# Kernel tuning notes

Measured on AMD Instinct MI355X. Metric: run time of the kernel, lower is better.

The kernel has to match this reference:

```python
import jax, jax.numpy as jnp
import numpy as np

N = 50000
E = 800000
NEG_SLOPE = 0.2


def gatv2_layer(x, src, dst, Wl, Wr, att, bias, heads, ch):
    # x: [N, Fin]; Wl/Wr: [Fin, heads*ch]; att: [heads, ch]; bias: [heads*ch]
    xl = (x @ Wl).reshape(N, heads, ch)  # source transform
    xr = (x @ Wr).reshape(N, heads, ch)  # target transform
    e = xl[src] + xr[dst]                              # [E, H, C]
    s = jnp.einsum('ehc,hc->eh', jax.nn.leaky_relu(e, NEG_SLOPE), att)  # [E, H]
    # scatter-softmax over incoming edges of each target node
    smax = jax.ops.segment_max(s, dst, num_segments=N)  # [N, H]
    ex = jnp.exp(s - smax[dst])
    denom = jax.ops.segment_sum(ex, dst, num_segments=N)
    alpha = ex / denom[dst]                             # [E, H]
    out = jax.ops.segment_sum(xl[src] * alpha[..., None], dst, num_segments=N)  # [N, H, C]
    return out.reshape(N, heads * ch) + bias


def setup_inputs() -> dict:
    key = jax.random.key(0)
    ks = jax.random.split(key, 12)
    x = jax.random.normal(ks[0], (N, 128), dtype=jnp.float32)
    edge_index = jax.random.randint(ks[1], (2, E), 0, N, dtype=jnp.int64)
    edge_attr = jax.random.normal(ks[2], (E, 16), dtype=jnp.float32)
    s1 = 1.0 / np.sqrt(128.0)
    # layer 1: 128 -> 64, heads=2 (concat -> 128)
    Wl1 = jax.random.normal(ks[3], (128, 128), dtype=jnp.float32) * s1
    Wr1 = jax.random.normal(ks[4], (128, 128), dtype=jnp.float32) * s1
    att1 = jax.random.normal(ks[5], (2, 64), dtype=jnp.float32) * 0.1
    b1 = jnp.zeros((128,), dtype=jnp.float32)
    # layer 2: 128 -> 128, heads=1
    Wl2 = jax.random.normal(ks[6], (128, 128), dtype=jnp.float32) * s1
    Wr2 = jax.random.normal(ks[7], (128, 128), dtype=jnp.float32) * s1
    att2 = jax.random.normal(ks[8], (1, 128), dtype=jnp.float32) * 0.1
    b2 = jnp.zeros((128,), dtype=jnp.float32)
    return {"x": x, "edge_index": edge_index, "edge_attr": edge_attr,
            "Wl1": Wl1, "Wr1": Wr1, "att1": att1, "b1": b1,
            "Wl2": Wl2, "Wr2": Wr2, "att2": att2, "b2": b2}


def reference(x, edge_index, edge_attr, Wl1, Wr1, att1, b1, Wl2, Wr2, att2, b2):
    # using_edge_attr=False default path: edge_attr ignored.
    # GATv2Conv default add_self_loops=True
    loops = jnp.arange(N, dtype=edge_index.dtype)
    src = jnp.concatenate([edge_index[0], loops])
    dst = jnp.concatenate([edge_index[1], loops])
    h = gatv2_layer(x, src, dst, Wl1, Wr1, att1, b1, heads=2, ch=64)
    out = gatv2_layer(h, src, dst, Wl2, Wr2, att2, b2, heads=1, ch=128)
    return out
```

## Files before the change

### kernel.cpp

```cpp
#include <hip/hip_runtime.h>

#define NEG_SLOPE 0.2f
#define NPB 256
#define CHUNK 4096

typedef _Float16 f16x8 __attribute__((ext_vector_type(8)));
typedef _Float16 f16x4 __attribute__((ext_vector_type(4)));
typedef _Float16 f16x2 __attribute__((ext_vector_type(2)));
typedef float    f32x4 __attribute__((ext_vector_type(4)));

__device__ __forceinline__ float lrelu(float v) { return fmaxf(v, NEG_SLOPE * v); }

__device__ __forceinline__ float4 ldf16x4(const _Float16* p) {
    f16x4 v = *(const f16x4*)p;
    return make_float4((float)v[0], (float)v[1], (float)v[2], (float)v[3]);
}

__global__ __launch_bounds__(256) void wsplit_kernel(
    const float* __restrict__ W0, const float* __restrict__ W1,
    const float* __restrict__ W2, const float* __restrict__ W3,
    _Float16* __restrict__ wt)
{
    int idx = blockIdx.x * 256 + threadIdx.x;
    int m = idx >> 14;
    int k = (idx >> 7) & 127;
    int n = idx & 127;
    const float* W = (m == 0) ? W0 : (m == 1) ? W1 : (m == 2) ? W2 : W3;
    wt[m * 16384 + n * 128 + k] = (_Float16)W[k * 128 + n];
}

__global__ __launch_bounds__(256) void xsplit_kernel(
    const float* __restrict__ x, _Float16* __restrict__ xh,
    _Float16* __restrict__ xlo, int total)
{
    int i = blockIdx.x * 256 + threadIdx.x;
    if (i * 2 < total) {
        float2 f = *(const float2*)(x + (size_t)i * 2);
        _Float16 h0 = (_Float16)f.x, h1 = (_Float16)f.y;
        _Float16 l0 = (_Float16)(f.x - (float)h0), l1 = (_Float16)(f.y - (float)h1);
        *(f16x2*)(xh  + (size_t)i * 2) = (f16x2){h0, h1};
        *(f16x2*)(xlo + (size_t)i * 2) = (f16x2){l0, l1};
    }
}

__global__ __launch_bounds__(256) void gemm_f16_kernel(
    const _Float16* __restrict__ Ahi, const _Float16* __restrict__ Alo,
    const _Float16* __restrict__ Wt0, const _Float16* __restrict__ Wt1,
    _Float16* __restrict__ Cl, float* __restrict__ Cr, int N)
{
    const _Float16* Wt = blockIdx.y ? Wt1 : Wt0;

    __shared__ _Float16 ldsW[128 * 136];

    const int tid = threadIdx.x;
    {
        int n = tid >> 1, hf = tid & 1;
        const float4* g = (const float4*)(Wt + n * 128 + hf * 64);
        float4* d = (float4*)&ldsW[n * 136 + hf * 64];
#pragma unroll
        for (int j = 0; j < 8; j++) d[j] = g[j];
    }

    const int wave = tid >> 6;
    const int lane = tid & 63;
    const int mrow = lane & 15;
    const int quad = lane >> 4;
    const int rbase = blockIdx.x * 128 + wave * 32;

    f16x8 ah[2][4], al[2][4];
#pragma unroll
    for (int rt = 0; rt < 2; rt++) {
        int r = rbase + rt * 16 + mrow;
        if (r > N - 1) r = N - 1;
        const _Float16* pa = Ahi + (size_t)r * 128 + quad * 8;
        const _Float16* pl = Alo + (size_t)r * 128 + quad * 8;
#pragma unroll
        for (int s = 0; s < 4; s++) {
            ah[rt][s] = *(const f16x8*)(pa + s * 32);
            al[rt][s] = *(const f16x8*)(pl + s * 32);
        }
    }

    f32x4 acc[2][8];
#pragma unroll
    for (int rt = 0; rt < 2; rt++)
#pragma unroll
        for (int c = 0; c < 8; c++) acc[rt][c] = (f32x4){0.f, 0.f, 0.f, 0.f};

    __syncthreads();

#pragma unroll
    for (int s = 0; s < 4; s++) {
#pragma unroll
        for (int c = 0; c < 8; c++) {
            f16x8 bw = *(const f16x8*)&ldsW[(c * 16 + mrow) * 136 + s * 32 + quad * 8];
            acc[0][c] = __builtin_amdgcn_mfma_f32_16x16x32_f16(ah[0][s], bw, acc[0][c], 0, 0, 0);
            acc[0][c] = __builtin_amdgcn_mfma_f32_16x16x32_f16(al[0][s], bw, acc[0][c], 0, 0, 0);
            acc[1][c] = __builtin_amdgcn_mfma_f32_16x16x32_f16(ah[1][s], bw, acc[1][c], 0, 0, 0);
            acc[1][c] = __builtin_amdgcn_mfma_f32_16x16x32_f16(al[1][s], bw, acc[1][c], 0, 0, 0);
        }
    }

    if (blockIdx.y == 0) {
#pragma unroll
        for (int rt = 0; rt < 2; rt++)
#pragma unroll
            for (int i = 0; i < 4; i++) {
                int r = rbase + rt * 16 + quad * 4 + i;
                if (r < N) {
                    _Float16* cr = Cl + (size_t)r * 128 + mrow;
#pragma unroll
                    for (int c = 0; c < 8; c++) cr[c * 16] = (_Float16)acc[rt][c][i];
                }
            }
    } else {
#pragma unroll
        for (int rt = 0; rt < 2; rt++)
#pragma unroll
            for (int i = 0; i < 4; i++) {
                int r = rbase + rt * 16 + quad * 4 + i;
                if (r < N) {
                    float* cr = Cr + (size_t)r * 128 + mrow;
#pragma unroll
                    for (int c = 0; c < 8; c++) cr[c * 16] = acc[rt][c][i];
                }
            }
    }
}

__global__ __launch_bounds__(256) void histB_kernel(
    const int* __restrict__ ei, int* __restrict__ bcnt, int E)
{
    __shared__ int bh[256];
    int t = threadIdx.x;
    bh[t] = 0;
    __syncthreads();
    int base = blockIdx.x * CHUNK;
#pragma unroll
    for (int j = 0; j < CHUNK / 256; j++) {
        int e = base + t + j * 256;
        if (e < E) atomicAdd(&bh[ei[E + e] >> 8], 1);
    }
    __syncthreads();
    if (bh[t]) atomicAdd(&bcnt[t], bh[t]);
}

__global__ __launch_bounds__(256) void scanB_kernel(
    const int* __restrict__ bcnt, int* __restrict__ bstart,
    int* __restrict__ gcursor, int NB, int E)
{
    __shared__ int s[256];
    int t = threadIdx.x;
    int v = (t < NB) ? bcnt[t] : 0;
    s[t] = v;
    __syncthreads();
    for (int off = 1; off < 256; off <<= 1) {
        int u = (t >= off) ? s[t - off] : 0;
        __syncthreads();
        s[t] += u;
        __syncthreads();
    }
    if (t < NB) { bstart[t] = s[t] - v; gcursor[t] = s[t] - v; }
    if (t == 0) bstart[NB] = E;
}

__global__ __launch_bounds__(256) void passA_kernel(
    const int* __restrict__ ei, int* __restrict__ gcursor,
    int2* __restrict__ staging, int E)
{
    __shared__ int bh[256];
    __shared__ int bbase[256];
    int t = threadIdx.x;
    bh[t] = 0;
    __syncthreads();
    int base = blockIdx.x * CHUNK;
    int srcv[16], dstv[16], rb[16];
#pragma unroll
    for (int j = 0; j < 16; j++) {
        int e = base + t + j * 256;
        if (e < E) {
            int d = ei[E + e];
            srcv[j] = ei[e];
            dstv[j] = d;
            int bk = d >> 8;
            int r = atomicAdd(&bh[bk], 1);
            rb[j] = (r << 8) | bk;
        } else rb[j] = -1;
    }
    __syncthreads();
    if (bh[t]) bbase[t] = atomicAdd(&gcursor[t], bh[t]);
    __syncthreads();
#pragma unroll
    for (int j = 0; j < 16; j++) {
        if (rb[j] >= 0) {
            int bk = rb[j] & 255, r = rb[j] >> 8;
            staging[bbase[bk] + r] = make_int2(srcv[j], dstv[j]);
        }
    }
}

__global__ __launch_bounds__(256) void passB_kernel(
    const int2* __restrict__ staging, const int* __restrict__ bstart,
    int* __restrict__ start, int* __restrict__ sorted_src, int N, int E)
{
    __shared__ int lhist[256], lscan[256], lcur[256];
    int b = blockIdx.x, t = threadIdx.x;
    int r0 = bstart[b], r1 = bstart[b + 1];
    lhist[t] = 0;
    __syncthreads();
    for (int i = r0 + t; i < r1; i += 256) atomicAdd(&lhist[staging[i].y & 255], 1);
    __syncthreads();
    int v = lhist[t];
    lscan[t] = v;
    __syncthreads();
    for (int off = 1; off < 256; off <<= 1) {
        int u = (t >= off) ? lscan[t - off] : 0;
        __syncthreads();
        lscan[t] += u;
        __syncthreads();
    }
    int excl = lscan[t] - v;
    int node = b * NPB + t;
    if (node < N) start[node] = r0 + excl;
    lcur[t] = excl;
    if (b == 0 && t == 0) start[N] = E;
    __syncthreads();
    for (int i = r0 + t; i < r1; i += 256) {
        int2 p = staging[i];
        int rank = atomicAdd(&lcur[p.y & 255], 1);
        sorted_src[r0 + rank] = p.x;
    }
}

template <int H, bool BFOUT>
__global__ __launch_bounds__(256) void gat_fused_kernel(
    const _Float16* __restrict__ xl, const float* __restrict__ xr,
    const float* __restrict__ att, const float* __restrict__ bias,
    const int* __restrict__ start, const int* __restrict__ sorted_src,
    float* __restrict__ outf, _Float16* __restrict__ oh,
    _Float16* __restrict__ ol, int N)
{
    int node = blockIdx.x * 4 + (threadIdx.x >> 6);
    if (node >= N) return;
    const int lane = threadIdx.x & 63;
    const int half = lane >> 5;
    const int hl   = lane & 31;
    const int RED  = (H == 2) ? 8 : 16;

    const float4 b  = *(const float4*)(xr + (size_t)node * 128 + hl * 4);
    const float4 av = *(const float4*)(att + hl * 4);

    float4 acc = make_float4(0.f, 0.f, 0.f, 0.f);
    float den = 0.f;

    const int s0 = start[node];
    const int s1 = start[node + 1];
    const int M  = s1 - s0 + 1;
    const int Ksafe = (M - 1) >> 1;
    const int K     = (M + 1) >> 1;

    int k = 0;
    for (; k + 4 <= Ksafe; k += 4) {
        int src[4];
#pragma unroll
        for (int j = 0; j < 4; j++) {
            int iv = 2 * (k + j) + half;
            src[j] = (iv == 0) ? node : sorted_src[s0 + iv - 1];
        }
        float4 a[4];
#pragma unroll
        for (int j = 0; j < 4; j++)
            a[j] = ldf16x4(xl + (size_t)src[j] * 128 + hl * 4);
        float p[4];
#pragma unroll
        for (int j = 0; j < 4; j++) {
            p[j] = lrelu(a[j].x + b.x) * av.x + lrelu(a[j].y + b.y) * av.y
                 + lrelu(a[j].z + b.z) * av.z + lrelu(a[j].w + b.w) * av.w;
        }
#pragma unroll
        for (int m = 1; m <= RED; m <<= 1) {
#pragma unroll
            for (int j = 0; j < 4; j++) p[j] += __shfl_xor(p[j], m, 64);
        }
#pragma unroll
        for (int j = 0; j < 4; j++) {
            float e = __expf(p[j]);
            den += e;
            acc.x += e * a[j].x; acc.y += e * a[j].y;
            acc.z += e * a[j].z; acc.w += e * a[j].w;
        }
    }
    for (; k < Ksafe; k++) {
        int iv = 2 * k + half;
        int src = (iv == 0) ? node : sorted_src[s0 + iv - 1];
        float4 a = ldf16x4(xl + (size_t)src * 128 + hl * 4);
        float p = lrelu(a.x + b.x) * av.x + lrelu(a.y + b.y) * av.y
                + lrelu(a.z + b.z) * av.z + lrelu(a.w + b.w) * av.w;
#pragma unroll
        for (int m = 1; m <= RED; m <<= 1) p += __shfl_xor(p, m, 64);
        float e = __expf(p);
        den += e;
        acc.x += e * a.x; acc.y += e * a.y; acc.z += e * a.z; acc.w += e * a.w;
    }
    for (; k < K; k++) {
        int iv = 2 * k + half;
        bool valid = iv < M;
        int pos = s0 + (iv > 0 ? iv - 1 : 0);
        int ld = sorted_src[pos];
        int src = (iv == 0) ? node : (valid ? ld : node);
        float4 a = ldf16x4(xl + (size_t)src * 128 + hl * 4);
        float p = lrelu(a.x + b.x) * av.x + lrelu(a.y + b.y) * av.y
                + lrelu(a.z + b.z) * av.z + lrelu(a.w + b.w) * av.w;
#pragma unroll
        for (int m = 1; m <= RED; m <<= 1) p += __shfl_xor(p, m, 64);
        float e = valid ? __expf(p) : 0.f;
        den += e;
        acc.x += e * a.x; acc.y += e * a.y; acc.z += e * a.z; acc.w += e * a.w;
    }

    den   += __shfl_xor(den,   32, 64);
    acc.x += __shfl_xor(acc.x, 32, 64);
    acc.y += __shfl_xor(acc.y, 32, 64);
    acc.z += __shfl_xor(acc.z, 32, 64);
    acc.w += __shfl_xor(acc.w, 32, 64);

    float inv = 1.0f / den;
    float4 bi = *(const float4*)(bias + hl * 4);
    float o0 = acc.x * inv + bi.x;
    float o1 = acc.y * inv + bi.y;
    float o2 = acc.z * inv + bi.z;
    float o3 = acc.w * inv + bi.w;

    if (lane < 32) {
        if (BFOUT) {
            _Float16 h0 = (_Float16)o0, h1 = (_Float16)o1, h2 = (_Float16)o2, h3 = (_Float16)o3;
            f16x4 hv = {h0, h1, h2, h3};
            f16x4 lv = {(_Float16)(o0 - (float)h0), (_Float16)(o1 - (float)h1),
                        (_Float16)(o2 - (float)h2), (_Float16)(o3 - (float)h3)};
            *(f16x4*)(oh + (size_t)node * 128 + hl * 4) = hv;
            *(f16x4*)(ol + (size_t)node * 128 + hl * 4) = lv;
        } else {
            *(float4*)(outf + (size_t)node * 128 + hl * 4) = make_float4(o0, o1, o2, o3);
        }
    }
}

extern "C" void kernel_launch(void* const* d_in, const int* in_sizes, int n_in,
                              void* d_out, int out_size, void* d_ws, size_t ws_size,
                              hipStream_t stream)
{
    const float* x    = (const float*)d_in[0];
    const int*   ei   = (const int*)d_in[1];
    const float* Wl1  = (const float*)d_in[3];
    const float* Wr1  = (const float*)d_in[4];
    const float* att1 = (const float*)d_in[5];
    const float* b1   = (const float*)d_in[6];
    const float* Wl2  = (const float*)d_in[7];
    const float* Wr2  = (const float*)d_in[8];
    const float* att2 = (const float*)d_in[9];
    const float* b2   = (const float*)d_in[10];
    float* out = (float*)d_out;

    const int N  = in_sizes[0] / 128;
    const int E  = in_sizes[1] / 2;
    const int NB = (N + NPB - 1) / NPB;

    const size_t nf = (size_t)N * 128;
    float* xr      = (float*)d_ws;
    _Float16* xlf  = (_Float16*)(xr + nf);
    _Float16* ah   = xlf + nf;
    _Float16* al   = ah + nf;
    _Float16* wt   = al + nf;
    int* bcnt      = (int*)(wt + 4 * 16384);
    int* bstart    = bcnt + 256;
    int* gcursor   = bstart + 257;
    int* start     = gcursor + 256;
    size_t stgoff  = ((size_t)(start + N + 1) + 7) & ~(size_t)7;
    int2* staging  = (int2*)stgoff;
    int* sorted_src = (int*)(staging + E);

    const int grid_chunk = (E + CHUNK - 1) / CHUNK;
    const int node_grid  = (N + 3) / 4;
    const int gemm_gx    = (N + 127) / 128;
    const int split_grid = (int)((nf / 2 + 255) / 256);

    wsplit_kernel<<<256, 256, 0, stream>>>(Wl1, Wr1, Wl2, Wr2, wt);
    xsplit_kernel<<<split_grid, 256, 0, stream>>>(x, ah, al, (int)nf);

    hipMemsetAsync(bcnt, 0, 256 * sizeof(int), stream);
    histB_kernel<<<grid_chunk, 256, 0, stream>>>(ei, bcnt, E);
    scanB_kernel<<<1, 256, 0, stream>>>(bcnt, bstart, gcursor, NB, E);
    passA_kernel<<<grid_chunk, 256, 0, stream>>>(ei, gcursor, staging, E);
    passB_kernel<<<NB, 256, 0, stream>>>(staging, bstart, start, sorted_src, N, E);

    gemm_f16_kernel<<<dim3(gemm_gx, 2), 256, 0, stream>>>(
        ah, al, wt + 0 * 16384, wt + 1 * 16384, xlf, xr, N);
    gat_fused_kernel<2, true><<<node_grid, 256, 0, stream>>>(
        xlf, xr, att1, b1, start, sorted_src, nullptr, ah, al, N);

    gemm_f16_kernel<<<dim3(gemm_gx, 2), 256, 0, stream>>>(
        ah, al, wt + 2 * 16384, wt + 3 * 16384, xlf, xr, N);
    gat_fused_kernel<1, false><<<node_grid, 256, 0, stream>>>(
        xlf, xr, att2, b2, start, sorted_src, out, nullptr, nullptr, N);
}
```

Before: 316.7 us.

## Store xr in fp16, compute scores with packed f16 dot, fuse prep kernels

Merges the weight-transpose, x hi/lo split and histogram memset into a single prep kernel. The GEMM now writes xr as fp16 instead of fp32 and loads weights into registers before the A-tile loads, so global latency overlaps. The attention kernel computes leaky-relu and the score dot product in packed fp16 using fdot2, folds log2(e) into att so exp2f can be used, and adds an 8-wide unrolled gather loop. This cuts launch count, xr memory traffic and ALU work, at the cost of reduced precision in the attention scores.

```diff
diff --git a/kernel.cpp b/kernel.cpp
--- a/kernel.cpp
+++ b/kernel.cpp
@@ -9,64 +9,69 @@
 typedef _Float16 f16x2 __attribute__((ext_vector_type(2)));
 typedef float    f32x4 __attribute__((ext_vector_type(4)));
 
-__device__ __forceinline__ float lrelu(float v) { return fmaxf(v, NEG_SLOPE * v); }
-
-__device__ __forceinline__ float4 ldf16x4(const _Float16* p) {
-    f16x4 v = *(const f16x4*)p;
-    return make_float4((float)v[0], (float)v[1], (float)v[2], (float)v[3]);
-}
-
-__global__ __launch_bounds__(256) void wsplit_kernel(
+#if defined(__has_builtin)
+#if __has_builtin(__builtin_amdgcn_fdot2)
+#define HAVE_FDOT2 1
+#endif
+#endif
+
+__device__ __forceinline__ f32x4 cvt4(f16x4 v) {
+    return __builtin_convertvector(v, f32x4);
+}
+
+__global__ __launch_bounds__(256) void prep_kernel(
     const float* __restrict__ W0, const float* __restrict__ W1,
     const float* __restrict__ W2, const float* __restrict__ W3,
-    _Float16* __restrict__ wt)
-{
-    int idx = blockIdx.x * 256 + threadIdx.x;
-    int m = idx >> 14;
-    int k = (idx >> 7) & 127;
-    int n = idx & 127;
-    const float* W = (m == 0) ? W0 : (m == 1) ? W1 : (m == 2) ? W2 : W3;
-    wt[m * 16384 + n * 128 + k] = (_Float16)W[k * 128 + n];
-}
-
-__global__ __launch_bounds__(256) void xsplit_kernel(
+    _Float16* __restrict__ wt,
     const float* __restrict__ x, _Float16* __restrict__ xh,
-    _Float16* __restrict__ xlo, int total)
-{
-    int i = blockIdx.x * 256 + threadIdx.x;
-    if (i * 2 < total) {
-        float2 f = *(const float2*)(x + (size_t)i * 2);
-        _Float16 h0 = (_Float16)f.x, h1 = (_Float16)f.y;
-        _Float16 l0 = (_Float16)(f.x - (float)h0), l1 = (_Float16)(f.y - (float)h1);
-        *(f16x2*)(xh  + (size_t)i * 2) = (f16x2){h0, h1};
-        *(f16x2*)(xlo + (size_t)i * 2) = (f16x2){l0, l1};
+    _Float16* __restrict__ xlo, int total, int* __restrict__ bcnt)
+{
+    int t = threadIdx.x;
+    if (blockIdx.x < 256) {
+        if (blockIdx.x == 0) bcnt[t] = 0;
+        int idx = blockIdx.x * 256 + t;
+        int m = idx >> 14;
+        int k = (idx >> 7) & 127;
+        int n = idx & 127;
+        const float* W = (m == 0) ? W0 : (m == 1) ? W1 : (m == 2) ? W2 : W3;
+        wt[m * 16384 + n * 128 + k] = (_Float16)W[k * 128 + n];
+    } else {
+        int i = (blockIdx.x - 256) * 256 + t;
+        if (i * 2 < total) {
+            float2 f = *(const float2*)(x + (size_t)i * 2);
+            _Float16 h0 = (_Float16)f.x, h1 = (_Float16)f.y;
+            _Float16 l0 = (_Float16)(f.x - (float)h0), l1 = (_Float16)(f.y - (float)h1);
+            *(f16x2*)(xh  + (size_t)i * 2) = (f16x2){h0, h1};
+            *(f16x2*)(xlo + (size_t)i * 2) = (f16x2){l0, l1};
+        }
     }
 }
 
 __global__ __launch_bounds__(256) void gemm_f16_kernel(
     const _Float16* __restrict__ Ahi, const _Float16* __restrict__ Alo,
     const _Float16* __restrict__ Wt0, const _Float16* __restrict__ Wt1,
-    _Float16* __restrict__ Cl, float* __restrict__ Cr, int N)
+    _Float16* __restrict__ Cl, _Float16* __restrict__ Cr, int N)
 {
     const _Float16* Wt = blockIdx.y ? Wt1 : Wt0;
+    _Float16* C = blockIdx.y ? Cr : Cl;
 
     __shared__ _Float16 ldsW[128 * 136];
 
     const int tid = threadIdx.x;
-    {
-        int n = tid >> 1, hf = tid & 1;
-        const float4* g = (const float4*)(Wt + n * 128 + hf * 64);
-        float4* d = (float4*)&ldsW[n * 136 + hf * 64];
-#pragma unroll
-        for (int j = 0; j < 8; j++) d[j] = g[j];
-    }
-
     const int wave = tid >> 6;
     const int lane = tid & 63;
     const int mrow = lane & 15;
     const int quad = lane >> 4;
     const int rbase = blockIdx.x * 128 + wave * 32;
 
+    const int sn = tid >> 1, shf = tid & 1;
+    float4 stg[8];
+    {
+        const float4* g = (const float4*)(Wt + sn * 128 + shf * 64);
+#pragma unroll
+        for (int j = 0; j < 8; j++) stg[j] = g[j];
+    }
+
     f16x8 ah[2][4], al[2][4];
 #pragma unroll
     for (int rt = 0; rt < 2; rt++) {
@@ -79,6 +84,12 @@
             ah[rt][s] = *(const f16x8*)(pa + s * 32);
             al[rt][s] = *(const f16x8*)(pl + s * 32);
         }
+    }
+
+    {
+        float4* d = (float4*)&ldsW[sn * 136 + shf * 64];
+#pragma unroll
+        for (int j = 0; j < 8; j++) d[j] = stg[j];
     }
 
     f32x4 acc[2][8];
@@ -101,31 +112,17 @@
         }
     }
 
-    if (blockIdx.y == 0) {
-#pragma unroll
-        for (int rt = 0; rt < 2; rt++)
-#pragma unroll
-            for (int i = 0; i < 4; i++) {
-                int r = rbase + rt * 16 + quad * 4 + i;
-                if (r < N) {
-                    _Float16* cr = Cl + (size_t)r * 128 + mrow;
-#pragma unroll
-                    for (int c = 0; c < 8; c++) cr[c * 16] = (_Float16)acc[rt][c][i];
-                }
+#pragma unroll
+    for (int rt = 0; rt < 2; rt++)
+#pragma unroll
+        for (int i = 0; i < 4; i++) {
+            int r = rbase + rt * 16 + quad * 4 + i;
+            if (r < N) {
+                _Float16* cr = C + (size_t)r * 128 + mrow;
+#pragma unroll
+                for (int c = 0; c < 8; c++) cr[c * 16] = (_Float16)acc[rt][c][i];
             }
-    } else {
-#pragma unroll
-        for (int rt = 0; rt < 2; rt++)
-#pragma unroll
-            for (int i = 0; i < 4; i++) {
-                int r = rbase + rt * 16 + quad * 4 + i;
-                if (r < N) {
-                    float* cr = Cr + (size_t)r * 128 + mrow;
-#pragma unroll
-                    for (int c = 0; c < 8; c++) cr[c * 16] = acc[rt][c][i];
-                }
-            }
-    }
+        }
 }
 
 __global__ __launch_bounds__(256) void histB_kernel(
@@ -234,7 +231,7 @@
 
 template <int H, bool BFOUT>
 __global__ __launch_bounds__(256) void gat_fused_kernel(
-    const _Float16* __restrict__ xl, const float* __restrict__ xr,
+    const _Float16* __restrict__ xl, const _Float16* __restrict__ xr,
     const float* __restrict__ att, const float* __restrict__ bias,
     const int* __restrict__ start, const int* __restrict__ sorted_src,
     float* __restrict__ outf, _Float16* __restrict__ oh,
@@ -246,11 +243,43 @@
     const int half = lane >> 5;
     const int hl   = lane & 31;
     const int RED  = (H == 2) ? 8 : 16;
-
-    const float4 b  = *(const float4*)(xr + (size_t)node * 128 + hl * 4);
-    const float4 av = *(const float4*)(att + hl * 4);
-
-    float4 acc = make_float4(0.f, 0.f, 0.f, 0.f);
+    const _Float16 NS = (_Float16)NEG_SLOPE;
+
+    const f16x4 b4 = *(const f16x4*)(xr + (size_t)node * 128 + hl * 4);
+    float4 attf = *(const float4*)(att + hl * 4);
+    const float L2E = 1.44269504f;
+    f16x4 av = {(_Float16)(attf.x * L2E), (_Float16)(attf.y * L2E),
+                (_Float16)(attf.z * L2E), (_Float16)(attf.w * L2E)};
+#if defined(HAVE_FDOT2)
+    f16x2 avlo = __builtin_shufflevector(av, av, 0, 1);
+    f16x2 avhi = __builtin_shufflevector(av, av, 2, 3);
+#else
+    f32x4 avf = cvt4(av);
+#endif
+
+#define SCORE(a_, p_) {                                                     \
+        f16x4 t_ = (a_) + b4;                                               \
+        f16x4 u_ = __builtin_elementwise_max(t_, t_ * NS);                  \
+        _Float16 dummy_;                                                    \
+        (void)dummy_;                                                       \
+                                                \
+        p_ = 0.f;                                                           \
+        score_dot(u_, p_);                                                  \
+    }
+
+    auto score_dot = [&](f16x4 u_, float& p_) {
+#if defined(HAVE_FDOT2)
+        f16x2 ulo = __builtin_shufflevector(u_, u_, 0, 1);
+        f16x2 uhi = __builtin_shufflevector(u_, u_, 2, 3);
+        p_ = __builtin_amdgcn_fdot2(ulo, avlo,
+             __builtin_amdgcn_fdot2(uhi, avhi, 0.0f, false), false);
+#else
+        f32x4 uf = cvt4(u_);
+        p_ = uf[0] * avf[0] + uf[1] * avf[1] + uf[2] * avf[2] + uf[3] * avf[3];
+#endif
+    };
+
+    f32x4 acc = (f32x4){0.f, 0.f, 0.f, 0.f};
     float den = 0.f;
 
     const int s0 = start[node];
@@ -260,47 +289,64 @@
     const int K     = (M + 1) >> 1;
 
     int k = 0;
+    for (; k + 8 <= Ksafe; k += 8) {
+        int src[8]; f16x4 a[8]; float p[8];
+#pragma unroll
+        for (int j = 0; j < 8; j++) {
+            int iv = 2 * (k + j) + half;
+            src[j] = (iv == 0) ? node : sorted_src[s0 + iv - 1];
+        }
+#pragma unroll
+        for (int j = 0; j < 8; j++)
+            a[j] = *(const f16x4*)(xl + (size_t)src[j] * 128 + hl * 4);
+#pragma unroll
+        for (int j = 0; j < 8; j++) SCORE(a[j], p[j]);
+#pragma unroll
+        for (int m = 1; m <= RED; m <<= 1) {
+#pragma unroll
+            for (int j = 0; j < 8; j++) p[j] += __shfl_xor(p[j], m, 64);
+        }
+#pragma unroll
+        for (int j = 0; j < 8; j++) {
+            float e = exp2f(p[j]);
+            den += e;
+            acc = acc + cvt4(a[j]) * e;
+        }
+    }
     for (; k + 4 <= Ksafe; k += 4) {
-        int src[4];
+        int src[4]; f16x4 a[4]; float p[4];
 #pragma unroll
         for (int j = 0; j < 4; j++) {
             int iv = 2 * (k + j) + half;
             src[j] = (iv == 0) ? node : sorted_src[s0 + iv - 1];
         }
-        float4 a[4];
 #pragma unroll
         for (int j = 0; j < 4; j++)
-            a[j] = ldf16x4(xl + (size_t)src[j] * 128 + hl * 4);
-        float p[4];
+            a[j] = *(const f16x4*)(xl + (size_t)src[j] * 128 + hl * 4);
+#pragma unroll
+        for (int j = 0; j < 4; j++) SCORE(a[j], p[j]);
+#pragma unroll
+        for (int m = 1; m <= RED; m <<= 1) {
+#pragma unroll
+            for (int j = 0; j < 4; j++) p[j] += __shfl_xor(p[j], m, 64);
+        }
 #pragma unroll
         for (int j = 0; j < 4; j++) {
-            p[j] = lrelu(a[j].x + b.x) * av.x + lrelu(a[j].y + b.y) * av.y
-                 + lrelu(a[j].z + b.z) * av.z + lrelu(a[j].w + b.w) * av.w;
-        }
-#pragma unroll
-        for (int m = 1; m <= RED; m <<= 1) {
-#pragma unroll
-            for (int j = 0; j < 4; j++) p[j] += __shfl_xor(p[j], m, 64);
-        }
-#pragma unroll
-        for (int j = 0; j < 4; j++) {
-            float e = __expf(p[j]);
+            float e = exp2f(p[j]);
             den += e;
-            acc.x += e * a[j].x; acc.y += e * a[j].y;
-            acc.z += e * a[j].z; acc.w += e * a[j].w;
+            acc = acc + cvt4(a[j]) * e;
         }
     }
     for (; k < Ksafe; k++) {
         int iv = 2 * k + half;
         int src = (iv == 0) ? node : sorted_src[s0 + iv - 1];
-        float4 a = ldf16x4(xl + (size_t)src * 128 + hl * 4);
-        float p = lrelu(a.x + b.x) * av.x + lrelu(a.y + b.y) * av.y
-                + lrelu(a.z + b.z) * av.z + lrelu(a.w + b.w) * av.w;
+        f16x4 a = *(const f16x4*)(xl + (size_t)src * 128 + hl * 4);
+        float p; SCORE(a, p);
 #pragma unroll
         for (int m = 1; m <= RED; m <<= 1) p += __shfl_xor(p, m, 64);
-        float e = __expf(p);
+        float e = exp2f(p);
         den += e;
-        acc.x += e * a.x; acc.y += e * a.y; acc.z += e * a.z; acc.w += e * a.w;
+        acc = acc + cvt4(a) * e;
     }
     for (; k < K; k++) {
         int iv = 2 * k + half;
@@ -308,28 +354,28 @@
         int pos = s0 + (iv > 0 ? iv - 1 : 0);
         int ld = sorted_src[pos];
         int src = (iv == 0) ? node : (valid ? ld : node);
-        float4 a = ldf16x4(xl + (size_t)src * 128 + hl * 4);
-        float p = lrelu(a.x + b.x) * av.x + lrelu(a.y + b.y) * av.y
-                + lrelu(a.z + b.z) * av.z + lrelu(a.w + b.w) * av.w;
+        f16x4 a = *(const f16x4*)(xl + (size_t)src * 128 + hl * 4);
+        float p; SCORE(a, p);
 #pragma unroll
         for (int m = 1; m <= RED; m <<= 1) p += __shfl_xor(p, m, 64);
-        float e = valid ? __expf(p) : 0.f;
+        float e = valid ? exp2f(p) : 0.f;
         den += e;
-        acc.x += e * a.x; acc.y += e * a.y; acc.z += e * a.z; acc.w += e * a.w;
-    }
-
-    den   += __shfl_xor(den,   32, 64);
-    acc.x += __shfl_xor(acc.x, 32, 64);
-    acc.y += __shfl_xor(acc.y, 32, 64);
-    acc.z += __shfl_xor(acc.z, 32, 64);
-    acc.w += __shfl_xor(acc.w, 32, 64);
+        acc = acc + cvt4(a) * e;
+    }
+#undef SCORE
+
+    den    += __shfl_xor(den,    32, 64);
+    acc[0] += __shfl_xor(acc[0], 32, 64);
+    acc[1] += __shfl_xor(acc[1], 32, 64);
+    acc[2] += __shfl_xor(acc[2], 32, 64);
+    acc[3] += __shfl_xor(acc[3], 32, 64);
 
     float inv = 1.0f / den;
     float4 bi = *(const float4*)(bias + hl * 4);
-    float o0 = acc.x * inv + bi.x;
-    float o1 = acc.y * inv + bi.y;
-    float o2 = acc.z * inv + bi.z;
-    float o3 = acc.w * inv + bi.w;
+    float o0 = acc[0] * inv + bi.x;
+    float o1 = acc[1] * inv + bi.y;
+    float o2 = acc[2] * inv + bi.z;
+    float o3 = acc[3] * inv + bi.w;
 
     if (lane < 32) {
         if (BFOUT) {
@@ -366,9 +412,9 @@
     const int NB = (N + NPB - 1) / NPB;
 
     const size_t nf = (size_t)N * 128;
-    float* xr      = (float*)d_ws;
-    _Float16* xlf  = (_Float16*)(xr + nf);
-    _Float16* ah   = xlf + nf;
+    _Float16* xlf  = (_Float16*)d_ws;
+    _Float16* xrf  = xlf + nf;
+    _Float16* ah   = xrf + nf;
     _Float16* al   = ah + nf;
     _Float16* wt   = al + nf;
     int* bcnt      = (int*)(wt + 4 * 16384);
@@ -384,22 +430,21 @@
     const int gemm_gx    = (N + 127) / 128;
     const int split_grid = (int)((nf / 2 + 255) / 256);
 
-    wsplit_kernel<<<256, 256, 0, stream>>>(Wl1, Wr1, Wl2, Wr2, wt);
-    xsplit_kernel<<<split_grid, 256, 0, stream>>>(x, ah, al, (int)nf);
-
-    hipMemsetAsync(bcnt, 0, 256 * sizeof(int), stream);
+    prep_kernel<<<256 + split_grid, 256, 0, stream>>>(
+        Wl1, Wr1, Wl2, Wr2, wt, x, ah, al, (int)nf, bcnt);
+
     histB_kernel<<<grid_chunk, 256, 0, stream>>>(ei, bcnt, E);
     scanB_kernel<<<1, 256, 0, stream>>>(bcnt, bstart, gcursor, NB, E);
     passA_kernel<<<grid_chunk, 256, 0, stream>>>(ei, gcursor, staging, E);
     passB_kernel<<<NB, 256, 0, stream>>>(staging, bstart, start, sorted_src, N, E);
 
     gemm_f16_kernel<<<dim3(gemm_gx, 2), 256, 0, stream>>>(
-        ah, al, wt + 0 * 16384, wt + 1 * 16384, xlf, xr, N);
+        ah, al, wt + 0 * 16384, wt + 1 * 16384, xlf, xrf, N);
     gat_fused_kernel<2, true><<<node_grid, 256, 0, stream>>>(
-        xlf, xr, att1, b1, start, sorted_src, nullptr, ah, al, N);
+        xlf, xrf, att1, b1, start, sorted_src, nullptr, ah, al, N);
 
     gemm_f16_kernel<<<dim3(gemm_gx, 2), 256, 0, stream>>>(
-        ah, al, wt + 2 * 16384, wt + 3 * 16384, xlf, xr, N);
+        ah, al, wt + 2 * 16384, wt + 3 * 16384, xlf, xrf, N);
     gat_fused_kernel<1, false><<<node_grid, 256, 0, stream>>>(
-        xlf, xr, att2, b2, start, sorted_src, out, nullptr, nullptr, N);
-}
+        xlf, xrf, att2, b2, start, sorted_src, out, nullptr, nullptr, N);
+}
```

Measured after the change: 305.7 us. -3.5%, faster.
